# Kernel optimization log

Hardware: AMD Instinct MI355X
Metric: run time of the kernel (lower is better)

Reference implementation:

```python
import jax, jax.numpy as jnp
import numpy as np

N1, N2 = 8192, 8192
E1, E2 = 131072, 131072
F_IN, NH, B = 64, 128, 256
D6 = 6 * NH  # set2set in_channels = 768


def _gcn(x, W, b, src, dst, ew, n):
    xw = x @ W
    loop = jnp.arange(n)
    s = jnp.concatenate([src, loop])
    d = jnp.concatenate([dst, loop])
    w = jnp.concatenate([ew, jnp.ones((n,), ew.dtype)])
    deg = jax.ops.segment_sum(w, d, num_segments=n)
    dinv = jnp.where(deg > 0, jax.lax.rsqrt(deg), 0.0)
    norm = (dinv[s] * w * dinv[d])[:, None]
    return jax.ops.segment_sum(xw[s] * norm, d, num_segments=n) + b


def _leaky(x):
    return jax.nn.leaky_relu(x, 0.2)


def _l2norm(x):
    return x / jnp.maximum(jnp.linalg.norm(x, axis=1, keepdims=True), 1e-12)


def _set2set(x, batch, nseg, Wih, Whh, bih, bhh, steps=2):
    # Set2Set pooling: LSTM(input=2d, hidden=d) + segment softmax attention
    d = x.shape[1]
    h = jnp.zeros((nseg, d), x.dtype)
    c = jnp.zeros((nseg, d), x.dtype)
    q_star = jnp.zeros((nseg, 2 * d), x.dtype)
    for _ in range(steps):
        gates = q_star @ Wih.T + h @ Whh.T + bih + bhh
        gi, gf, gg, go = jnp.split(gates, 4, axis=1)  # torch LSTM gate order i,f,g,o
        c = jax.nn.sigmoid(gf) * c + jax.nn.sigmoid(gi) * jnp.tanh(gg)
        h = jax.nn.sigmoid(go) * jnp.tanh(c)
        e = jnp.sum(x * h[batch], axis=1)
        emax = jax.ops.segment_max(e, batch, num_segments=nseg)
        ee = jnp.exp(e - emax[batch])
        a = ee / jax.ops.segment_sum(ee, batch, num_segments=nseg)[batch]
        r = jax.ops.segment_sum(a[:, None] * x, batch, num_segments=nseg)
        q_star = jnp.concatenate([h, r], axis=1)
    return q_star


def setup_inputs():
    key = jax.random.key(0)
    ks = jax.random.split(key, 20)
    f32 = jnp.float32

    def xav(k, shp):
        fan_in, fan_out = shp[-1], shp[0] if len(shp) == 2 else shp[-1]
        lim = float(np.sqrt(6.0 / (shp[0] + shp[1])))
        return jax.random.uniform(k, shp, f32, -lim, lim)

    inp = {}
    inp["features_1"] = jax.random.normal(ks[0], (N1, F_IN), f32)
    inp["features_2"] = jax.random.normal(ks[1], (N2, F_IN), f32)
    inp["edge_attr_1"] = jax.random.uniform(ks[2], (E1,), f32)
    inp["edge_attr_2"] = jax.random.uniform(ks[3], (E2,), f32)
    inp["W0"] = xav(ks[4], (F_IN, NH)); inp["b0"] = jnp.zeros((NH,), f32)
    inp["W1"] = xav(ks[5], (NH, NH)); inp["b1"] = jnp.zeros((NH,), f32)
    inp["W2"] = xav(ks[6], (NH, NH)); inp["b2"] = jnp.zeros((NH,), f32)
    inp["Wih"] = xav(ks[7], (4 * D6, 2 * D6)); inp["bih"] = jnp.zeros((4 * D6,), f32)
    inp["Whh"] = xav(ks[8], (4 * D6, D6)); inp["bhh"] = jnp.zeros((4 * D6,), f32)
    inp["Wp1"] = xav(ks[9], (256, 4 * D6)); inp["bp1"] = jnp.zeros((256,), f32)
    inp["Wp2"] = xav(ks[10], (128, 256)); inp["bp2"] = jnp.zeros((128,), f32)
    inp["Wp3"] = xav(ks[11], (1, 128)); inp["bp3"] = jnp.zeros((1,), f32)
    inp["edge_index_1"] = jax.random.randint(ks[12], (2, E1), 0, N1)
    inp["edge_index_2"] = jax.random.randint(ks[13], (2, E2), 0, N2)
    inp["batch_1"] = jnp.sort(jax.random.randint(ks[14], (N1,), 0, B))
    inp["batch_2"] = jnp.sort(jax.random.randint(ks[15], (N2,), 0, B))
    return inp


def reference(features_1, features_2, edge_attr_1, edge_attr_2,
              W0, b0, W1, b1, W2, b2, Wih, bih, Whh, bhh,
              Wp1, bp1, Wp2, bp2, Wp3, bp3,
              edge_index_1, edge_index_2, batch_1, batch_2):
    s1, d1 = edge_index_1[0], edge_index_1[1]
    s2, d2 = edge_index_2[0], edge_index_2[1]

    f1a = _leaky(_gcn(features_1, W0, b0, s1, d1, edge_attr_1, N1))
    f2a = _leaky(_gcn(features_2, W0, b0, s2, d2, edge_attr_2, N2))
    f1b = _leaky(_gcn(f1a, W1, b1, s1, d1, edge_attr_1, N1))
    f2b = _leaky(_gcn(f2a, W1, b1, s2, d2, edge_attr_2, N2))
    f1c = _leaky(_gcn(f1b, W2, b2, s1, d1, edge_attr_1, N1))
    f2c = _leaky(_gcn(f2b, W2, b2, s2, d2, edge_attr_2, N2))
    h1 = jnp.concatenate([f1a, f1b, f1c], axis=1)  # [N1, 3*NH]
    h2 = jnp.concatenate([f2a, f2b, f2c], axis=1)  # [N2, 3*NH]

    # interaction: cosine-sim map masked to same-graph pairs (len_map)
    ns = _l2norm(h1)
    nv = _l2norm(h2)
    mask = (batch_1[:, None] == batch_2[None, :]).astype(ns.dtype)  # [N1, N2]
    imap = (ns @ nv.T) * mask
    f1 = jnp.concatenate([ns, imap @ nv], axis=1)      # [N1, 6*NH]
    f2 = jnp.concatenate([nv, imap.T @ ns], axis=1)    # [N2, 6*NH]

    g1 = _set2set(f1, batch_1, B, Wih, Whh, bih, bhh)  # [B, 12*NH]
    g2 = _set2set(f2, batch_2, B, Wih, Whh, bih, bhh)  # [B, 12*NH]
    z = jnp.concatenate([g1, g2], axis=1)              # [B, 24*NH]
    z = jax.nn.relu(z @ Wp1.T + bp1)
    z = jax.nn.relu(z @ Wp2.T + bp2)
    z = z @ Wp3.T + bp3
    return jax.nn.sigmoid(z).reshape(-1)
```

## Files before the change

kernel.cpp:

```cpp
#include <hip/hip_runtime.h>
#include <cmath>

#define N_NODES 8192
#define N_EDGES 131072
#define NB      256
#define NH      128
#define D3      384
#define D6      768
#define SMM     96

typedef __attribute__((ext_vector_type(8))) short short8v;
typedef __attribute__((ext_vector_type(4))) float f32x4;
typedef unsigned short bf16t;

__device__ __forceinline__ float sigf(float x){ return 1.0f/(1.0f+__expf(-x)); }
__device__ __forceinline__ unsigned short f2bf(float x){
  unsigned u = __float_as_uint(x);
  unsigned r = u + 0x7FFF + ((u>>16)&1);
  return (unsigned short)(r>>16);
}
__device__ __forceinline__ float bfl(unsigned u){ return __uint_as_float(u<<16); }
__device__ __forceinline__ float bfh(unsigned u){ return __uint_as_float(u & 0xFFFF0000u); }
__device__ __forceinline__ float b2f(bf16t u){ return __uint_as_float(((unsigned)u)<<16); }
__device__ __forceinline__ float h0val(const float* bih, const float* bhh, int j){
  float c = sigf(bih[j]+bhh[j]) * tanhf(bih[2*D6+j]+bhh[2*D6+j]);
  return sigf(bih[3*D6+j]+bhh[3*D6+j]) * tanhf(c);
}


__global__ void k_init(float* deg1, float* deg2, int* ecnt1, int* ecnt2, int* cnt1, int* cnt2){
  int t = blockIdx.x*blockDim.x + threadIdx.x;
  if (t < N_NODES){ deg1[t]=1.f; deg2[t]=1.f; ecnt1[t]=0; ecnt2[t]=0; }
  if (t < NB){ cnt1[t]=0; cnt2[t]=0; }
}

__global__ void k_deg(const int* __restrict__ ei1, const float* __restrict__ ea1, float* deg1, int* ecnt1,
                      const int* __restrict__ ei2, const float* __restrict__ ea2, float* deg2, int* ecnt2,
                      const int* __restrict__ b1, const int* __restrict__ b2, int* cnt1, int* cnt2){
  int idx = blockIdx.x*blockDim.x + threadIdx.x;
  int side = idx >= N_EDGES;
  int e = idx & (N_EDGES-1);
  const int* ei = side? ei2:ei1; const float* ea = side? ea2:ea1;
  float* deg = side? deg2:deg1;  int* ecnt = side? ecnt2:ecnt1;
  int d = ei[N_EDGES+e];
  atomicAdd(&deg[d], ea[e]);
  atomicAdd(&ecnt[d], 1);
  if (idx < N_NODES){ atomicAdd(&cnt1[b1[idx]],1); atomicAdd(&cnt2[b2[idx]],1); }
}

__global__ __launch_bounds__(256) void k_scan256(const int* c1, const int* c2, int* s1, int* s2){
  const int* c = blockIdx.x? c2:c1; int* st = blockIdx.x? s2:s1;
  __shared__ int ps[256];
  int t = threadIdx.x;
  ps[t]=c[t]; __syncthreads();
  for (int d=1; d<256; d<<=1){
    int v = (t>=d)? ps[t-d]:0;
    __syncthreads();
    ps[t]+=v;
    __syncthreads();
  }
  st[t+1]=ps[t];
  if (t==0) st[0]=0;
}

__global__ __launch_bounds__(1024) void k_escan(const int* ec1, const int* ec2,
                                                int* off1, int* cur1, int* off2, int* cur2){
  const int* cnt = blockIdx.x? ec2:ec1;
  int* off = blockIdx.x? off2:off1;
  int* cur = blockIdx.x? cur2:cur1;
  __shared__ int ps[1024];
  int t = threadIdx.x;
  int base = t*8;
  int loc[8]; int s=0;
  #pragma unroll
  for (int k=0;k<8;k++){ loc[k]=s; s+=cnt[base+k]; }
  ps[t]=s; __syncthreads();
  for (int d=1; d<1024; d<<=1){
    int v = (t>=d)? ps[t-d]:0;
    __syncthreads();
    ps[t]+=v;
    __syncthreads();
  }
  int pre = (t==0)? 0 : ps[t-1];
  #pragma unroll
  for (int k=0;k<8;k++){ int v=pre+loc[k]; off[base+k]=v; cur[base+k]=v; }
  if (t==1023) off[N_NODES]=ps[1023];
}

__global__ void k_fill(const int* __restrict__ ei1, const float* __restrict__ ea1, const float* __restrict__ d1,
                       int* cur1, int* es1, float* ec1,
                       const int* __restrict__ ei2, const float* __restrict__ ea2, const float* __restrict__ d2,
                       int* cur2, int* es2, float* ec2){
  int idx = blockIdx.x*blockDim.x + threadIdx.x;
  int side = idx >= N_EDGES;
  int e = idx & (N_EDGES-1);
  const int* ei = side? ei2:ei1; const float* ea = side? ea2:ea1;
  const float* deg = side? d2:d1;
  int* cur = side? cur2:cur1; int* es = side? es2:es1; float* ec = side? ec2:ec1;
  int s = ei[e], d = ei[N_EDGES+e];
  int pos = atomicAdd(&cur[d], 1);
  es[pos] = s;
  ec[pos] = rsqrtf(deg[s])*ea[e]*rsqrtf(deg[d]);
}

__global__ __launch_bounds__(256) void k_setup(
    const float* __restrict__ Wih, short* __restrict__ Wih16,
    const float* __restrict__ Wp1, short* __restrict__ Wp116,
    const float* __restrict__ fe1, const float* __restrict__ fe2,
    short* __restrict__ xf1, short* __restrict__ xf2,
    const float* __restrict__ W0, const float* __restrict__ W1, const float* __restrict__ W2,
    bf16t* __restrict__ Wt, uint4* __restrict__ Sz,
    const float* __restrict__ Whh, const float* __restrict__ bih, const float* __restrict__ bhh,
    float* __restrict__ cvec){
  __shared__ float hs[D6];
  int b = blockIdx.x, tid = threadIdx.x;
  if (b < 2304){
    int t = b*256 + tid;
    int n = t/192, q = t - n*192;
    float4 v = ((const float4*)(Wih + (size_t)n*1536 + 768))[q];
    short4 o = { (short)f2bf(v.x), (short)f2bf(v.y), (short)f2bf(v.z), (short)f2bf(v.w) };
    ((short4*)Wih16)[t] = o;
  } else if (b < 3072){
    int t = (b-2304)*256 + tid;
    float4 v = ((const float4*)Wp1)[t];
    short4 o = { (short)f2bf(v.x), (short)f2bf(v.y), (short)f2bf(v.z), (short)f2bf(v.w) };
    ((short4*)Wp116)[t] = o;
  } else if (b < 4096){
    int t = (b-3072)*256 + tid;
    int side = t >= 131072; int i = t & 131071;
    float4 v = ((const float4*)(side? fe2:fe1))[i];
    short4 o = { (short)f2bf(v.x), (short)f2bf(v.y), (short)f2bf(v.z), (short)f2bf(v.w) };
    ((short4*)(side? xf2:xf1))[i] = o;
  } else if (b < 6400){
    Sz[(size_t)(b-4096)*256 + tid] = make_uint4(0,0,0,0);
  } else if (b < 6403){
    int l = b - 6400;
    const float* W = (l==0)? W0 : ((l==1)? W1 : W2);
    int K = (l==0)? 64 : 128;
    bf16t* dst = Wt + ((l==0)? 0 : ((l==1)? 128*64 : 128*64+128*128));
    for (int idx = tid; idx < 128*K; idx += 256){
      int n = idx / K, k = idx - n*K;
      dst[idx] = f2bf(W[k*NH + n]);
    }
  } else {
    int j0 = (b - 6403)*4;
    for (int k=tid; k<D6; k+=256) hs[k] = h0val(bih,bhh,k);
    __syncthreads();
    int w = tid>>6, lane = tid&63;
    int j = j0 + w;
    const float4* wi = (const float4*)(Wih + (size_t)j*(2*D6));
    const float4* wh = (const float4*)(Whh + (size_t)j*D6);
    const float4* h4 = (const float4*)hs;
    float acc=0;
    #pragma unroll
    for (int m=0;m<3;m++){
      float4 hv = h4[m*64+lane];
      float4 a = wi[m*64+lane];
      float4 bb = wh[m*64+lane];
      acc += hv.x*(a.x+bb.x) + hv.y*(a.y+bb.y) + hv.z*(a.z+bb.z) + hv.w*(a.w+bb.w);
    }
    #pragma unroll
    for (int m=1;m<64;m<<=1) acc += __shfl_xor(acc,m,64);
    if (lane==0) cvec[j]=acc+bih[j]+bhh[j];
  }
}


__global__ __launch_bounds__(256) void k_xw_mfma(const bf16t* __restrict__ x1, const bf16t* __restrict__ x2,
                                                 int xs, int K, const bf16t* __restrict__ Wt,
                                                 bf16t* __restrict__ xw1, bf16t* __restrict__ xw2){
  int blk = blockIdx.x;
  int side = blk >> 8; int b = blk & 255;
  const bf16t* x = side? x2:x1;
  bf16t* xw = side? xw2:xw1;
  int w = threadIdx.x>>6, lane = threadIdx.x&63;
  int lm = lane&15, quad = lane>>4;
  int r0 = b*32 + (w>>1)*16;
  int c0 = (w&1)*64;
  const bf16t* a = x + (size_t)(r0+lm)*xs + quad*8;
  f32x4 acc[4] = {};
  for (int k=0;k<K;k+=32){
    short8v af = *(const short8v*)(a + k);
    #pragma unroll
    for (int ni=0;ni<4;ni++){
      short8v bf = *(const short8v*)(Wt + (size_t)(c0+ni*16+lm)*K + quad*8 + k);
      acc[ni] = __builtin_amdgcn_mfma_f32_16x16x32_bf16(af, bf, acc[ni], 0,0,0);
    }
  }
  #pragma unroll
  for (int ni=0;ni<4;ni++)
    #pragma unroll
    for (int r=0;r<4;r++){
      int row = r0 + quad*4 + r, col = c0 + ni*16 + lm;
      xw[(size_t)row*NH + col] = f2bf(acc[ni][r]);
    }
}

__global__ __launch_bounds__(256) void k_gather(const bf16t* __restrict__ xw1, const bf16t* __restrict__ xw2,
                                                const int* __restrict__ off1, const int* __restrict__ off2,
                                                const int* __restrict__ es1, const int* __restrict__ es2,
                                                const float* __restrict__ ec1, const float* __restrict__ ec2,
                                                const float* __restrict__ d1, const float* __restrict__ d2,
                                                const float* __restrict__ b,
                                                bf16t* __restrict__ h1, bf16t* __restrict__ h2, int loff,
                                                int l2mode, bf16t* __restrict__ f1, bf16t* __restrict__ f2){
  int blk = blockIdx.x;
  int side = blk >> 10; int bb = blk & 1023;
  const ushort4* xw = (const ushort4*)(side? xw2:xw1);
  const int* off = side? off2:off1;
  const int* es  = side? es2:es1;
  const float* ec= side? ec2:ec1;
  const float* deg = side? d2:d1;
  bf16t* h = side? h2:h1;
  int t = threadIdx.x;
  int i = bb*8 + (t>>5);
  int c4 = t & 31;
  float sc = 1.0f/deg[i];
  ushort4 v = xw[(size_t)i*32 + c4];
  float4 acc = {b2f(v.x)*sc, b2f(v.y)*sc, b2f(v.z)*sc, b2f(v.w)*sc};
  int r = off[i], r1 = off[i+1];
  for (; r+3<r1; r+=4){
    int s0=es[r], s1=es[r+1], s2=es[r+2], s3=es[r+3];
    float w0=ec[r], w1=ec[r+1], w2=ec[r+2], w3=ec[r+3];
    ushort4 u0 = xw[(size_t)s0*32 + c4];
    ushort4 u1 = xw[(size_t)s1*32 + c4];
    ushort4 u2 = xw[(size_t)s2*32 + c4];
    ushort4 u3 = xw[(size_t)s3*32 + c4];
    acc.x += b2f(u0.x)*w0 + b2f(u1.x)*w1 + b2f(u2.x)*w2 + b2f(u3.x)*w3;
    acc.y += b2f(u0.y)*w0 + b2f(u1.y)*w1 + b2f(u2.y)*w2 + b2f(u3.y)*w3;
    acc.z += b2f(u0.z)*w0 + b2f(u1.z)*w1 + b2f(u2.z)*w2 + b2f(u3.z)*w3;
    acc.w += b2f(u0.w)*w0 + b2f(u1.w)*w1 + b2f(u2.w)*w2 + b2f(u3.w)*w3;
  }
  for (; r<r1; r++){
    int s0=es[r]; float w0=ec[r];
    ushort4 u0 = xw[(size_t)s0*32 + c4];
    acc.x+=b2f(u0.x)*w0; acc.y+=b2f(u0.y)*w0; acc.z+=b2f(u0.z)*w0; acc.w+=b2f(u0.w)*w0;
  }
  float4 bv = ((const float4*)b)[c4];
  acc.x+=bv.x; acc.y+=bv.y; acc.z+=bv.z; acc.w+=bv.w;
  acc.x = (acc.x>0.f)?acc.x:0.2f*acc.x;
  acc.y = (acc.y>0.f)?acc.y:0.2f*acc.y;
  acc.z = (acc.z>0.f)?acc.z:0.2f*acc.z;
  acc.w = (acc.w>0.f)?acc.w:0.2f*acc.w;
  if (!l2mode){
    ((ushort4*)(h + (size_t)i*D3 + loff))[c4] =
      make_ushort4(f2bf(acc.x), f2bf(acc.y), f2bf(acc.z), f2bf(acc.w));
  } else {
    ushort4 u0 = ((const ushort4*)(h + (size_t)i*D3))[c4];
    ushort4 u1 = ((const ushort4*)(h + (size_t)i*D3 + 128))[c4];
    float4 v0 = {b2f(u0.x), b2f(u0.y), b2f(u0.z), b2f(u0.w)};
    float4 v1 = {b2f(u1.x), b2f(u1.y), b2f(u1.z), b2f(u1.w)};
    float ss = v0.x*v0.x+v0.y*v0.y+v0.z*v0.z+v0.w*v0.w
             + v1.x*v1.x+v1.y*v1.y+v1.z*v1.z+v1.w*v1.w
             + acc.x*acc.x+acc.y*acc.y+acc.z*acc.z+acc.w*acc.w;
    #pragma unroll
    for (int m=1;m<32;m<<=1) ss += __shfl_xor(ss, m, 64);
    float scale = 1.0f/fmaxf(sqrtf(ss), 1e-12f);
    bf16t* f = side? f2:f1;
    ((ushort4*)(f + (size_t)i*D6))[c4]       = make_ushort4(f2bf(v0.x*scale),f2bf(v0.y*scale),f2bf(v0.z*scale),f2bf(v0.w*scale));
    ((ushort4*)(f + (size_t)i*D6 + 128))[c4] = make_ushort4(f2bf(v1.x*scale),f2bf(v1.y*scale),f2bf(v1.z*scale),f2bf(v1.w*scale));
    ((ushort4*)(f + (size_t)i*D6 + 256))[c4] = make_ushort4(f2bf(acc.x*scale),f2bf(acc.y*scale),f2bf(acc.z*scale),f2bf(acc.w*scale));
  }
}

__global__ __launch_bounds__(256) void k_smat(const bf16t* __restrict__ f1, const bf16t* __restrict__ f2,
                                              const int* __restrict__ st1, const int* __restrict__ st2,
                                              bf16t* __restrict__ S, bf16t* __restrict__ ST){
  int g = blockIdx.x;
  int it2 = blockIdx.y/3, jt2 = blockIdx.y - it2*3;
  int i0 = st1[g]; int n1 = st1[g+1]-i0; if (n1>SMM) n1=SMM;
  int j0 = st2[g]; int n2 = st2[g+1]-j0; if (n2>SMM) n2=SMM;
  if (it2*32 >= n1 || jt2*32 >= n2) return;
  int w = threadIdx.x >> 6, lane = threadIdx.x & 63;
  int lm = lane & 15, quad = lane >> 4;
  int ti = it2*2 + (w>>1), tj = jt2*2 + (w&1);
  if (ti*16 >= n1 || tj*16 >= n2) return;
  const bf16t* a = f1 + (size_t)(i0 + ti*16 + lm)*D6 + quad*8;
  const bf16t* b = f2 + (size_t)(j0 + tj*16 + lm)*D6 + quad*8;
  f32x4 acc = {0,0,0,0};
  #pragma unroll
  for (int k=0; k<384; k+=32){
    short8v af = *(const short8v*)(a + k);
    short8v bf = *(const short8v*)(b + k);
    acc = __builtin_amdgcn_mfma_f32_16x16x32_bf16(af, bf, acc, 0, 0, 0);
  }
  bf16t* Sg  = S  + (size_t)g*SMM*SMM;
  bf16t* STg = ST + (size_t)g*SMM*SMM;
  int col = tj*16 + lm;
  #pragma unroll
  for (int r=0;r<4;r++){
    int row = ti*16 + quad*4 + r;
    if (row < n1 && col < n2){
      bf16t v = f2bf(acc[r]);
      Sg [(size_t)row*SMM + col] = v;
      STg[(size_t)col*SMM + row] = v;
    }
  }
}

__global__ __launch_bounds__(256) void k_apply(bf16t* __restrict__ f1, bf16t* __restrict__ f2,
                                               const int* __restrict__ st1, const int* __restrict__ st2,
                                               const bf16t* __restrict__ S, const bf16t* __restrict__ ST){
  __shared__ bf16t tbuf[32*392];
  int bx = blockIdx.x;
  int side = bx >> 8, g = bx & (NB-1);
  int a0 = st1[g]; int n1 = st1[g+1]-a0; if (n1>SMM) n1=SMM;
  int b0 = st2[g]; int n2 = st2[g+1]-b0; if (n2>SMM) n2=SMM;
  int cnt = side? n2 : n1;
  int J   = side? n1 : n2;
  int r0 = blockIdx.y*32;
  if (r0 >= cnt) return;
  const bf16t* src = side? (f1 + (size_t)a0*D6) : (f2 + (size_t)b0*D6);
  bf16t* dst = (side? (f2 + (size_t)b0*D6) : (f1 + (size_t)a0*D6)) + D3;
  const bf16t* Sg = (side? ST : S) + (size_t)g*SMM*SMM;
  int t = threadIdx.x, w = t>>6, lane = t&63;
  int lm = lane & 15, quad = lane >> 4;
  int mt1 = (cnt - r0 > 16) ? 2 : 1;
  f32x4 acc[2][6] = {};
  for (int kb = 0; kb < J; kb += 32){
    __syncthreads();
    for (int idx = t; idx < 32*48; idx += 256){
      int j = idx/48, cg = idx - j*48;
      uint4 v = (kb+j < J)? ((const uint4*)(src + (size_t)(kb+j)*D6))[cg] : make_uint4(0,0,0,0);
      *(uint4*)(tbuf + j*392 + cg*8) = v;
    }
    short8v af0, af1;
    {
      const bf16t* ap = Sg + (size_t)(r0 + lm)*SMM + kb + quad*8;
      af0 = *(const short8v*)ap;
      af1 = (mt1 > 1)? *(const short8v*)(ap + 16*SMM) : af0;
    }
    __syncthreads();
    #pragma unroll
    for (int ni = 0; ni < 6; ni++){
      int nt = w*6 + ni;
      short8v bf;
      #pragma unroll
      for (int ji = 0; ji < 8; ji++)
        bf[ji] = (short)tbuf[(quad*8 + ji)*392 + nt*16 + lm];
      acc[0][ni] = __builtin_amdgcn_mfma_f32_16x16x32_bf16(af0, bf, acc[0][ni], 0, 0, 0);
      if (mt1 > 1)
        acc[1][ni] = __builtin_amdgcn_mfma_f32_16x16x32_bf16(af1, bf, acc[1][ni], 0, 0, 0);
    }
  }
  for (int mt = 0; mt < mt1; mt++)
    for (int ni = 0; ni < 6; ni++){
      int nt = w*6 + ni;
      #pragma unroll
      for (int r = 0; r < 4; r++){
        int row = r0 + mt*16 + quad*4 + r;
        if (row < cnt) dst[(size_t)row*D6 + nt*16 + lm] = f2bf(acc[mt][ni][r]);
      }
    }
}


__global__ __launch_bounds__(256) void k_att(const bf16t* __restrict__ f1, const bf16t* __restrict__ f2,
                                             const float* __restrict__ hbase, int perseg,
                                             const float* __restrict__ bih, const float* __restrict__ bhh,
                                             const int* __restrict__ st1, const int* __restrict__ st2,
                                             bf16t* __restrict__ dst16, long sidestep, long dstride){
  __shared__ float4 hs[192];
  __shared__ float e_s[SMM];
  __shared__ float part[4][D6];
  int side = blockIdx.x >> 8, g = blockIdx.x & (NB-1);
  const int* st = side? st2:st1;
  int n0 = st[g]; int cnt = st[g+1]-n0; if (cnt>SMM) cnt=SMM;
  const bf16t* x = (side? f2:f1) + (size_t)n0*D6;
  int t = threadIdx.x, w = t>>6, lane = t&63;
  if (t<192){
    if (perseg){
      hs[t] = ((const float4*)(hbase + (size_t)(side*NB+g)*D6))[t];
    } else {
      int j = t*4;
      hs[t] = make_float4(h0val(bih,bhh,j), h0val(bih,bhh,j+1), h0val(bih,bhh,j+2), h0val(bih,bhh,j+3));
    }
  }
  __syncthreads();
  for (int n=w; n<cnt; n+=4){
    const uint2* xr = (const uint2*)(x + (size_t)n*D6);
    float p = 0;
    #pragma unroll
    for (int m=0;m<3;m++){
      uint2 rv = xr[m*64+lane];
      float4 hvv = hs[m*64+lane];
      p += bfl(rv.x)*hvv.x + bfh(rv.x)*hvv.y + bfl(rv.y)*hvv.z + bfh(rv.y)*hvv.w;
    }
    #pragma unroll
    for (int m=1;m<64;m<<=1) p += __shfl_xor(p,m,64);
    if (lane==0) e_s[n]=p;
  }
  __syncthreads();
  if (w==0){
    float mx=-INFINITY;
    for (int n=lane;n<cnt;n+=64) mx=fmaxf(mx,e_s[n]);
    #pragma unroll
    for (int m=1;m<64;m<<=1) mx=fmaxf(mx,__shfl_xor(mx,m,64));
    float s=0;
    for (int n=lane;n<cnt;n+=64) s+=__expf(e_s[n]-mx);
    #pragma unroll
    for (int m=1;m<64;m<<=1) s+=__shfl_xor(s,m,64);
    float inv=1.0f/s;
    for (int n=lane;n<cnt;n+=64) e_s[n]=__expf(e_s[n]-mx)*inv;
  }
  __syncthreads();
  float av[3][4] = {};
  for (int n=w; n<cnt; n+=4){
    float a = e_s[n];
    const uint2* xr = (const uint2*)(x + (size_t)n*D6);
    #pragma unroll
    for (int m=0;m<3;m++){
      uint2 rv = xr[m*64+lane];
      av[m][0]+=a*bfl(rv.x); av[m][1]+=a*bfh(rv.x); av[m][2]+=a*bfl(rv.y); av[m][3]+=a*bfh(rv.y);
    }
  }
  #pragma unroll
  for (int m=0;m<3;m++)
    *(float4*)&part[w][(m*64+lane)*4] = make_float4(av[m][0],av[m][1],av[m][2],av[m][3]);
  __syncthreads();
  if (t<192){
    float4 p0 = *(const float4*)&part[0][t*4];
    float4 p1 = *(const float4*)&part[1][t*4];
    float4 p2 = *(const float4*)&part[2][t*4];
    float4 p3 = *(const float4*)&part[3][t*4];
    float4 s = make_float4(p0.x+p1.x+p2.x+p3.x, p0.y+p1.y+p2.y+p3.y,
                           p0.z+p1.z+p2.z+p3.z, p0.w+p1.w+p2.w+p3.w);
    ushort4 o = make_ushort4(f2bf(s.x), f2bf(s.y), f2bf(s.z), f2bf(s.w));
    ((ushort4*)(dst16 + side*sidestep + (size_t)g*dstride))[t]=o;
  }
}

__global__ __launch_bounds__(256) void k_gemm_mfma(const short* __restrict__ A16,
                                                   const short* __restrict__ B16,
                                                   float* __restrict__ pout){
  int w = threadIdx.x >> 6, lane = threadIdx.x & 63;
  int lm = lane & 15, quad = lane >> 4;
  int bm = blockIdx.x * 16;
  int bn = blockIdx.y * 256 + w * 64;
  const short* a = A16 + (size_t)(bm + lm)*768 + quad*8;
  const short* b = B16 + (size_t)(bn + lm)*768 + quad*8;
  f32x4 acc0={0,0,0,0}, acc1={0,0,0,0}, acc2={0,0,0,0}, acc3={0,0,0,0};
  for (int k=0; k<768; k+=32){
    short8v af = *(const short8v*)(a + k);
    short8v b0 = *(const short8v*)(b + k);
    short8v b1 = *(const short8v*)(b + 16*768 + k);
    short8v b2 = *(const short8v*)(b + 32*768 + k);
    short8v b3 = *(const short8v*)(b + 48*768 + k);
    acc0 = __builtin_amdgcn_mfma_f32_16x16x32_bf16(af, b0, acc0, 0, 0, 0);
    acc1 = __builtin_amdgcn_mfma_f32_16x16x32_bf16(af, b1, acc1, 0, 0, 0);
    acc2 = __builtin_amdgcn_mfma_f32_16x16x32_bf16(af, b2, acc2, 0, 0, 0);
    acc3 = __builtin_amdgcn_mfma_f32_16x16x32_bf16(af, b3, acc3, 0, 0, 0);
  }
  #pragma unroll
  for (int r=0;r<4;r++){
    size_t base = (size_t)(bm + quad*4 + r)*3072 + bn + lm;
    pout[base]      = acc0[r];
    pout[base + 16] = acc1[r];
    pout[base + 32] = acc2[r];
    pout[base + 48] = acc3[r];
  }
}

__global__ __launch_bounds__(256) void k_gemm_mfma_p1(const short* __restrict__ A16,
                                                      const short* __restrict__ B16,
                                                      float* __restrict__ pout){
  int w = threadIdx.x >> 6, lane = threadIdx.x & 63;
  int lm = lane & 15, quad = lane >> 4;
  int bm = blockIdx.x * 16;
  int bn = w * 64;
  int kbase = blockIdx.y * 192;
  const short* a = A16 + (size_t)(bm + lm)*3072 + quad*8 + kbase;
  const short* b = B16 + (size_t)(bn + lm)*3072 + quad*8 + kbase;
  f32x4 acc0={0,0,0,0}, acc1={0,0,0,0}, acc2={0,0,0,0}, acc3={0,0,0,0};
  for (int k=0; k<192; k+=32){
    short8v af = *(const short8v*)(a + k);
    short8v b0 = *(const short8v*)(b + k);
    short8v b1 = *(const short8v*)(b + 16*3072 + k);
    short8v b2 = *(const short8v*)(b + 32*3072 + k);
    short8v b3 = *(const short8v*)(b + 48*3072 + k);
    acc0 = __builtin_amdgcn_mfma_f32_16x16x32_bf16(af, b0, acc0, 0, 0, 0);
    acc1 = __builtin_amdgcn_mfma_f32_16x16x32_bf16(af, b1, acc1, 0, 0, 0);
    acc2 = __builtin_amdgcn_mfma_f32_16x16x32_bf16(af, b2, acc2, 0, 0, 0);
    acc3 = __builtin_amdgcn_mfma_f32_16x16x32_bf16(af, b3, acc3, 0, 0, 0);
  }
  float* po = pout + (size_t)blockIdx.y*256*256;
  #pragma unroll
  for (int r=0;r<4;r++){
    size_t base = (size_t)(bm + quad*4 + r)*256 + bn + lm;
    po[base]      = acc0[r];
    po[base + 16] = acc1[r];
    po[base + 32] = acc2[r];
    po[base + 48] = acc3[r];
  }
}

__global__ __launch_bounds__(256) void k_lstm_red(const float* __restrict__ pbuf,
                                                  const float* __restrict__ cvec,
                                                  const float* __restrict__ bih, const float* __restrict__ bhh,
                                                  float* __restrict__ h1s, bf16t* __restrict__ z16){
  int t = blockIdx.x*256 + threadIdx.x;
  int m = t/D6, j = t - m*D6;
  const float* p0 = pbuf + (size_t)m*3072 + j;
  float g4[4];
  #pragma unroll
  for (int q=0;q<4;q++) g4[q] = cvec[q*D6 + j] + p0[q*D6];
  float c0j = sigf(bih[j]+bhh[j]) * tanhf(bih[2*D6+j]+bhh[2*D6+j]);
  float c = sigf(g4[1])*c0j + sigf(g4[0])*tanhf(g4[2]);
  float h = sigf(g4[3])*tanhf(c);
  h1s[(size_t)m*D6 + j] = h;
  int side = m>>8, g = m&255;
  z16[(size_t)g*3072 + side*1536 + j] = f2bf(h);
}

__global__ __launch_bounds__(128) void k_p23(const float* __restrict__ pbuf, const float* __restrict__ bp1,
                                             const float* __restrict__ Wp2, const float* __restrict__ bp2,
                                             const float* __restrict__ Wp3, const float* __restrict__ bp3,
                                             float* __restrict__ out){
  __shared__ float zr[256];
  __shared__ float ws[2];
  int m = blockIdx.x, t = threadIdx.x;
  float2 zacc = ((const float2*)(bp1))[t];
  #pragma unroll
  for (int p=0;p<16;p++){
    float2 v = ((const float2*)(pbuf + (size_t)p*256*256 + (size_t)m*256))[t];
    zacc.x += v.x; zacc.y += v.y;
  }
  zr[2*t]   = fmaxf(zacc.x, 0.f);
  zr[2*t+1] = fmaxf(zacc.y, 0.f);
  __syncthreads();
  const float4* wrow = (const float4*)(Wp2 + (size_t)t*256);
  const float4* z4 = (const float4*)zr;
  float acc = bp2[t];
  #pragma unroll 8
  for (int k=0;k<64;k++){
    float4 wv = wrow[k], zv = z4[k];
    acc += wv.x*zv.x + wv.y*zv.y + wv.z*zv.z + wv.w*zv.w;
  }
  float p = fmaxf(acc,0.f)*Wp3[t];
  #pragma unroll
  for (int o=32;o;o>>=1) p += __shfl_down(p,o,64);
  if ((t&63)==0) ws[t>>6]=p;
  __syncthreads();
  if (t==0){ float v=ws[0]+ws[1]+bp3[0]; out[m]=1.0f/(1.0f+__expf(-v)); }
}


extern "C" void kernel_launch(void* const* d_in, const int* in_sizes, int n_in,
                              void* d_out, int out_size, void* d_ws, size_t ws_size,
                              hipStream_t stream){
  const float* feat1=(const float*)d_in[0];
  const float* feat2=(const float*)d_in[1];
  const float* ea1  =(const float*)d_in[2];
  const float* ea2  =(const float*)d_in[3];
  const float* W0=(const float*)d_in[4];  const float* b0=(const float*)d_in[5];
  const float* W1=(const float*)d_in[6];  const float* b1=(const float*)d_in[7];
  const float* W2=(const float*)d_in[8];  const float* b2=(const float*)d_in[9];
  const float* Wih=(const float*)d_in[10]; const float* bih=(const float*)d_in[11];
  const float* Whh=(const float*)d_in[12]; const float* bhh=(const float*)d_in[13];
  const float* Wp1=(const float*)d_in[14]; const float* bp1=(const float*)d_in[15];
  const float* Wp2=(const float*)d_in[16]; const float* bp2=(const float*)d_in[17];
  const float* Wp3=(const float*)d_in[18]; const float* bp3=(const float*)d_in[19];
  const int* ei1=(const int*)d_in[20]; const int* ei2=(const int*)d_in[21];
  const int* batch1=(const int*)d_in[22]; const int* batch2=(const int*)d_in[23];
  float* out = (float*)d_out;

  float* base = (float*)d_ws;
  size_t off = 0;
  auto alloc = [&](size_t n)->float* { float* r = base + off; off += (n + 255) & ~(size_t)255; return r; };
  float* deg1 = alloc(N_NODES);          float* deg2 = alloc(N_NODES);
  bf16t* xw1  = (bf16t*)alloc((size_t)N_NODES*NH/2);
  bf16t* xw2  = (bf16t*)alloc((size_t)N_NODES*NH/2);
  bf16t* hb1  = (bf16t*)alloc((size_t)N_NODES*D3/2);
  bf16t* hb2  = (bf16t*)alloc((size_t)N_NODES*D3/2);
  bf16t* xf1  = (bf16t*)alloc((size_t)N_NODES*64/2);
  bf16t* xf2  = (bf16t*)alloc((size_t)N_NODES*64/2);
  bf16t* Wtb  = (bf16t*)alloc((size_t)(128*64 + 2*128*128)/2);
  bf16t* f1   = (bf16t*)alloc((size_t)N_NODES*D6/2);
  bf16t* f2   = (bf16t*)alloc((size_t)N_NODES*D6/2);
  float* ecoef1 = alloc(N_EDGES);        float* ecoef2 = alloc(N_EDGES);
  float* cvec = alloc(4*D6);
  bf16t* Sbuf = (bf16t*)alloc((size_t)NB*SMM*SMM);
  bf16t* STbuf= Sbuf + (size_t)NB*SMM*SMM;
  float* h1s  = alloc((size_t)512*D6);
  bf16t* zbuf16 = (bf16t*)alloc((size_t)256*3072/2);
  float* pbuf = alloc((size_t)4*512*3072);
  short* Abuf16 = (short*)alloc((size_t)512*D6/2);
  short* Wih16  = (short*)alloc((size_t)3072*D6/2);
  short* Wp116  = (short*)alloc((size_t)256*3072/2);
  int* cnt1 = (int*)alloc(NB);   int* cnt2 = (int*)alloc(NB);
  int* st1  = (int*)alloc(NB+1); int* st2  = (int*)alloc(NB+1);
  int* ecnt1= (int*)alloc(N_NODES); int* ecnt2 = (int*)alloc(N_NODES);
  int* eoff1= (int*)alloc(N_NODES+1); int* eoff2 = (int*)alloc(N_NODES+1);
  int* ecur1= (int*)alloc(N_NODES); int* ecur2 = (int*)alloc(N_NODES);
  int* esrc1= (int*)alloc(N_EDGES); int* esrc2 = (int*)alloc(N_EDGES);
  (void)ws_size; (void)in_sizes; (void)n_in; (void)out_size;

  k_init   <<<32,256,0,stream>>>(deg1,deg2,ecnt1,ecnt2,cnt1,cnt2);
  k_deg    <<<1024,256,0,stream>>>(ei1,ea1,deg1,ecnt1, ei2,ea2,deg2,ecnt2, batch1,batch2,cnt1,cnt2);
  k_scan256<<<2,256,0,stream>>>(cnt1,cnt2,st1,st2);
  k_escan  <<<2,1024,0,stream>>>(ecnt1,ecnt2,eoff1,ecur1,eoff2,ecur2);
  k_fill   <<<1024,256,0,stream>>>(ei1,ea1,deg1,ecur1,esrc1,ecoef1, ei2,ea2,deg2,ecur2,esrc2,ecoef2);
  k_setup  <<<7171,256,0,stream>>>(Wih,Wih16, Wp1,Wp116, feat1,feat2,(short*)xf1,(short*)xf2,
                                   W0,W1,W2,Wtb, (uint4*)Sbuf, Whh,bih,bhh, cvec);

  const float* bs[3]={b0,b1,b2};
  const bf16t* Wts[3]={Wtb, Wtb+128*64, Wtb+128*64+128*128};
  for (int l=0;l<3;l++){
    const bf16t* x1 = (l==0)? xf1 : (hb1 + (l-1)*NH);
    const bf16t* x2 = (l==0)? xf2 : (hb2 + (l-1)*NH);
    int xs = (l==0)? 64 : D3;
    int K  = (l==0)? 64 : NH;
    k_xw_mfma<<<512,256,0,stream>>>(x1,x2,xs,K,Wts[l],xw1,xw2);
    k_gather <<<2048,256,0,stream>>>(xw1,xw2,eoff1,eoff2,esrc1,esrc2,ecoef1,ecoef2,
                                     deg1,deg2,bs[l],hb1,hb2,l*NH,(l==2)?1:0,f1,f2);
  }

  k_smat  <<<dim3(256,9),256,0,stream>>>(f1,f2,st1,st2,Sbuf,STbuf);
  k_apply <<<dim3(512,3),256,0,stream>>>(f1,f2,st1,st2,Sbuf,STbuf);

  k_att<<<512,256,0,stream>>>(f1,f2,(const float*)nullptr,0,bih,bhh,st1,st2,
                              (bf16t*)Abuf16,(long)256*D6,(long)D6);

  k_gemm_mfma<<<dim3(32,12),256,0,stream>>>(Abuf16, Wih16, pbuf);
  k_lstm_red <<<1536,256,0,stream>>>(pbuf,cvec,bih,bhh,h1s,zbuf16);

  k_att<<<512,256,0,stream>>>(f1,f2,h1s,1,bih,bhh,st1,st2,
                              zbuf16+768,(long)1536,(long)3072);

  k_gemm_mfma_p1<<<dim3(16,16),256,0,stream>>>((const short*)zbuf16, Wp116, pbuf);
  k_p23 <<<256,128,0,stream>>>(pbuf, bp1, Wp2, bp2, Wp3, bp3, out);
}
```

Before: 357.0 us.

## Fuse similarity and apply kernels, gates GEMM with LSTM, and setup launches

The per-graph similarity matrix is now computed into LDS and applied in the same kernel, for both sides. This drops the global S/ST buffers and the pass that zeroed them. The LSTM gate nonlinearity is applied in the GEMM epilogue through shared memory, so the full fp32 gate buffer is no longer written and reread. The init kernel is folded into the setup kernel and the two scans are merged into one launch, cutting launch count. The risk is that the fused interaction kernel runs only 256 blocks and handles both sides serially, so it has much less parallelism than the old split kernels.

```diff
diff --git a/kernel.cpp b/kernel.cpp
--- a/kernel.cpp
+++ b/kernel.cpp
@@ -8,6 +8,7 @@
 #define D3      384
 #define D6      768
 #define SMM     96
+#define SLD     104
 
 typedef __attribute__((ext_vector_type(8))) short short8v;
 typedef __attribute__((ext_vector_type(4))) float f32x4;
@@ -27,12 +28,6 @@
   return sigf(bih[3*D6+j]+bhh[3*D6+j]) * tanhf(c);
 }
 
-
-__global__ void k_init(float* deg1, float* deg2, int* ecnt1, int* ecnt2, int* cnt1, int* cnt2){
-  int t = blockIdx.x*blockDim.x + threadIdx.x;
-  if (t < N_NODES){ deg1[t]=1.f; deg2[t]=1.f; ecnt1[t]=0; ecnt2[t]=0; }
-  if (t < NB){ cnt1[t]=0; cnt2[t]=0; }
-}
 
 __global__ void k_deg(const int* __restrict__ ei1, const float* __restrict__ ea1, float* deg1, int* ecnt1,
                       const int* __restrict__ ei2, const float* __restrict__ ea2, float* deg2, int* ecnt2,
@@ -48,43 +43,43 @@
   if (idx < N_NODES){ atomicAdd(&cnt1[b1[idx]],1); atomicAdd(&cnt2[b2[idx]],1); }
 }
 
-__global__ __launch_bounds__(256) void k_scan256(const int* c1, const int* c2, int* s1, int* s2){
-  const int* c = blockIdx.x? c2:c1; int* st = blockIdx.x? s2:s1;
-  __shared__ int ps[256];
-  int t = threadIdx.x;
-  ps[t]=c[t]; __syncthreads();
-  for (int d=1; d<256; d<<=1){
-    int v = (t>=d)? ps[t-d]:0;
+__global__ __launch_bounds__(1024) void k_scans(const int* ec1, const int* ec2,
+                                                int* off1, int* cur1, int* off2, int* cur2,
+                                                const int* c1, const int* c2, int* s1, int* s2){
+  __shared__ int ps[1024];
+  int bx = blockIdx.x, t = threadIdx.x;
+  if (bx < 2){
+    const int* cnt = bx? ec2:ec1;
+    int* off = bx? off2:off1;
+    int* cur = bx? cur2:cur1;
+    int base = t*8;
+    int loc[8]; int s=0;
+    #pragma unroll
+    for (int k=0;k<8;k++){ loc[k]=s; s+=cnt[base+k]; }
+    ps[t]=s; __syncthreads();
+    for (int d=1; d<1024; d<<=1){
+      int v = (t>=d)? ps[t-d]:0;
+      __syncthreads();
+      ps[t]+=v;
+      __syncthreads();
+    }
+    int pre = (t==0)? 0 : ps[t-1];
+    #pragma unroll
+    for (int k=0;k<8;k++){ int v=pre+loc[k]; off[base+k]=v; cur[base+k]=v; }
+    if (t==1023) off[N_NODES]=ps[1023];
+  } else {
+    const int* c = (bx==3)? c2:c1; int* st = (bx==3)? s2:s1;
+    ps[t] = (t<256)? c[t] : 0;
     __syncthreads();
-    ps[t]+=v;
-    __syncthreads();
-  }
-  st[t+1]=ps[t];
-  if (t==0) st[0]=0;
-}
-
-__global__ __launch_bounds__(1024) void k_escan(const int* ec1, const int* ec2,
-                                                int* off1, int* cur1, int* off2, int* cur2){
-  const int* cnt = blockIdx.x? ec2:ec1;
-  int* off = blockIdx.x? off2:off1;
-  int* cur = blockIdx.x? cur2:cur1;
-  __shared__ int ps[1024];
-  int t = threadIdx.x;
-  int base = t*8;
-  int loc[8]; int s=0;
-  #pragma unroll
-  for (int k=0;k<8;k++){ loc[k]=s; s+=cnt[base+k]; }
-  ps[t]=s; __syncthreads();
-  for (int d=1; d<1024; d<<=1){
-    int v = (t>=d)? ps[t-d]:0;
-    __syncthreads();
-    ps[t]+=v;
-    __syncthreads();
-  }
-  int pre = (t==0)? 0 : ps[t-1];
-  #pragma unroll
-  for (int k=0;k<8;k++){ int v=pre+loc[k]; off[base+k]=v; cur[base+k]=v; }
-  if (t==1023) off[N_NODES]=ps[1023];
+    for (int d=1; d<256; d<<=1){
+      int v = (t>=d)? ps[t-d]:0;
+      __syncthreads();
+      ps[t]+=v;
+      __syncthreads();
+    }
+    if (t<256) st[t+1]=ps[t];
+    if (t==0) st[0]=0;
+  }
 }
 
 __global__ void k_fill(const int* __restrict__ ei1, const float* __restrict__ ea1, const float* __restrict__ d1,
@@ -109,9 +104,10 @@
     const float* __restrict__ fe1, const float* __restrict__ fe2,
     short* __restrict__ xf1, short* __restrict__ xf2,
     const float* __restrict__ W0, const float* __restrict__ W1, const float* __restrict__ W2,
-    bf16t* __restrict__ Wt, uint4* __restrict__ Sz,
+    bf16t* __restrict__ Wt,
     const float* __restrict__ Whh, const float* __restrict__ bih, const float* __restrict__ bhh,
-    float* __restrict__ cvec){
+    float* __restrict__ cvec,
+    float* deg1, float* deg2, int* ecnt1, int* ecnt2, int* cnt1, int* cnt2){
   __shared__ float hs[D6];
   int b = blockIdx.x, tid = threadIdx.x;
   if (b < 2304){
@@ -131,10 +127,8 @@
     float4 v = ((const float4*)(side? fe2:fe1))[i];
     short4 o = { (short)f2bf(v.x), (short)f2bf(v.y), (short)f2bf(v.z), (short)f2bf(v.w) };
     ((short4*)(side? xf2:xf1))[i] = o;
-  } else if (b < 6400){
-    Sz[(size_t)(b-4096)*256 + tid] = make_uint4(0,0,0,0);
-  } else if (b < 6403){
-    int l = b - 6400;
+  } else if (b < 4099){
+    int l = b - 4096;
     const float* W = (l==0)? W0 : ((l==1)? W1 : W2);
     int K = (l==0)? 64 : 128;
     bf16t* dst = Wt + ((l==0)? 0 : ((l==1)? 128*64 : 128*64+128*128));
@@ -142,8 +136,8 @@
       int n = idx / K, k = idx - n*K;
       dst[idx] = f2bf(W[k*NH + n]);
     }
-  } else {
-    int j0 = (b - 6403)*4;
+  } else if (b < 4867){
+    int j0 = (b - 4099)*4;
     for (int k=tid; k<D6; k+=256) hs[k] = h0val(bih,bhh,k);
     __syncthreads();
     int w = tid>>6, lane = tid&63;
@@ -162,6 +156,10 @@
     #pragma unroll
     for (int m=1;m<64;m<<=1) acc += __shfl_xor(acc,m,64);
     if (lane==0) cvec[j]=acc+bih[j]+bhh[j];
+  } else {
+    int t = (b-4867)*256 + tid;
+    if (t < N_NODES){ deg1[t]=1.f; deg2[t]=1.f; ecnt1[t]=0; ecnt2[t]=0; }
+    if (t < NB){ cnt1[t]=0; cnt2[t]=0; }
   }
 }
 
@@ -263,95 +261,91 @@
   }
 }
 
-__global__ __launch_bounds__(256) void k_smat(const bf16t* __restrict__ f1, const bf16t* __restrict__ f2,
-                                              const int* __restrict__ st1, const int* __restrict__ st2,
-                                              bf16t* __restrict__ S, bf16t* __restrict__ ST){
+__global__ __launch_bounds__(256) void k_inter(bf16t* __restrict__ f1, bf16t* __restrict__ f2,
+                                               const int* __restrict__ st1, const int* __restrict__ st2){
+  __shared__ bf16t Sld[SMM*SLD];
+  __shared__ bf16t STld[SMM*SLD];
+  __shared__ bf16t tbuf[32*392];
   int g = blockIdx.x;
-  int it2 = blockIdx.y/3, jt2 = blockIdx.y - it2*3;
   int i0 = st1[g]; int n1 = st1[g+1]-i0; if (n1>SMM) n1=SMM;
   int j0 = st2[g]; int n2 = st2[g+1]-j0; if (n2>SMM) n2=SMM;
-  if (it2*32 >= n1 || jt2*32 >= n2) return;
-  int w = threadIdx.x >> 6, lane = threadIdx.x & 63;
-  int lm = lane & 15, quad = lane >> 4;
-  int ti = it2*2 + (w>>1), tj = jt2*2 + (w&1);
-  if (ti*16 >= n1 || tj*16 >= n2) return;
-  const bf16t* a = f1 + (size_t)(i0 + ti*16 + lm)*D6 + quad*8;
-  const bf16t* b = f2 + (size_t)(j0 + tj*16 + lm)*D6 + quad*8;
-  f32x4 acc = {0,0,0,0};
-  #pragma unroll
-  for (int k=0; k<384; k+=32){
-    short8v af = *(const short8v*)(a + k);
-    short8v bf = *(const short8v*)(b + k);
-    acc = __builtin_amdgcn_mfma_f32_16x16x32_bf16(af, bf, acc, 0, 0, 0);
-  }
-  bf16t* Sg  = S  + (size_t)g*SMM*SMM;
-  bf16t* STg = ST + (size_t)g*SMM*SMM;
-  int col = tj*16 + lm;
-  #pragma unroll
-  for (int r=0;r<4;r++){
-    int row = ti*16 + quad*4 + r;
-    if (row < n1 && col < n2){
-      bf16t v = f2bf(acc[r]);
-      Sg [(size_t)row*SMM + col] = v;
-      STg[(size_t)col*SMM + row] = v;
-    }
-  }
-}
-
-__global__ __launch_bounds__(256) void k_apply(bf16t* __restrict__ f1, bf16t* __restrict__ f2,
-                                               const int* __restrict__ st1, const int* __restrict__ st2,
-                                               const bf16t* __restrict__ S, const bf16t* __restrict__ ST){
-  __shared__ bf16t tbuf[32*392];
-  int bx = blockIdx.x;
-  int side = bx >> 8, g = bx & (NB-1);
-  int a0 = st1[g]; int n1 = st1[g+1]-a0; if (n1>SMM) n1=SMM;
-  int b0 = st2[g]; int n2 = st2[g+1]-b0; if (n2>SMM) n2=SMM;
-  int cnt = side? n2 : n1;
-  int J   = side? n1 : n2;
-  int r0 = blockIdx.y*32;
-  if (r0 >= cnt) return;
-  const bf16t* src = side? (f1 + (size_t)a0*D6) : (f2 + (size_t)b0*D6);
-  bf16t* dst = (side? (f2 + (size_t)b0*D6) : (f1 + (size_t)a0*D6)) + D3;
-  const bf16t* Sg = (side? ST : S) + (size_t)g*SMM*SMM;
   int t = threadIdx.x, w = t>>6, lane = t&63;
   int lm = lane & 15, quad = lane >> 4;
-  int mt1 = (cnt - r0 > 16) ? 2 : 1;
-  f32x4 acc[2][6] = {};
-  for (int kb = 0; kb < J; kb += 32){
-    __syncthreads();
-    for (int idx = t; idx < 32*48; idx += 256){
-      int j = idx/48, cg = idx - j*48;
-      uint4 v = (kb+j < J)? ((const uint4*)(src + (size_t)(kb+j)*D6))[cg] : make_uint4(0,0,0,0);
-      *(uint4*)(tbuf + j*392 + cg*8) = v;
-    }
-    short8v af0, af1;
-    {
-      const bf16t* ap = Sg + (size_t)(r0 + lm)*SMM + kb + quad*8;
-      af0 = *(const short8v*)ap;
-      af1 = (mt1 > 1)? *(const short8v*)(ap + 16*SMM) : af0;
-    }
-    __syncthreads();
-    #pragma unroll
-    for (int ni = 0; ni < 6; ni++){
-      int nt = w*6 + ni;
-      short8v bf;
-      #pragma unroll
-      for (int ji = 0; ji < 8; ji++)
-        bf[ji] = (short)tbuf[(quad*8 + ji)*392 + nt*16 + lm];
-      acc[0][ni] = __builtin_amdgcn_mfma_f32_16x16x32_bf16(af0, bf, acc[0][ni], 0, 0, 0);
-      if (mt1 > 1)
-        acc[1][ni] = __builtin_amdgcn_mfma_f32_16x16x32_bf16(af1, bf, acc[1][ni], 0, 0, 0);
-    }
-  }
-  for (int mt = 0; mt < mt1; mt++)
-    for (int ni = 0; ni < 6; ni++){
-      int nt = w*6 + ni;
-      #pragma unroll
-      for (int r = 0; r < 4; r++){
-        int row = r0 + mt*16 + quad*4 + r;
-        if (row < cnt) dst[(size_t)row*D6 + nt*16 + lm] = f2bf(acc[mt][ni][r]);
+  {
+    uint4* z1 = (uint4*)Sld; uint4* z2 = (uint4*)STld;
+    uint4 zz = make_uint4(0,0,0,0);
+    for (int i=t; i<1248; i+=256){ z1[i]=zz; z2[i]=zz; }
+  }
+  __syncthreads();
+  int nti = (n1+15)>>4, ntj = (n2+15)>>4;
+  for (int tile = w; tile < nti*ntj; tile += 4){
+    int ti = tile/ntj, tj = tile - ti*ntj;
+    int ar = i0 + ti*16 + lm; if (ar > N_NODES-1) ar = N_NODES-1;
+    int br = j0 + tj*16 + lm; if (br > N_NODES-1) br = N_NODES-1;
+    const bf16t* a = f1 + (size_t)ar*D6 + quad*8;
+    const bf16t* b = f2 + (size_t)br*D6 + quad*8;
+    f32x4 acc = {0,0,0,0};
+    #pragma unroll
+    for (int k=0; k<384; k+=32){
+      short8v af = *(const short8v*)(a + k);
+      short8v bf = *(const short8v*)(b + k);
+      acc = __builtin_amdgcn_mfma_f32_16x16x32_bf16(af, bf, acc, 0, 0, 0);
+    }
+    int col = tj*16 + lm;
+    #pragma unroll
+    for (int r=0;r<4;r++){
+      int row = ti*16 + quad*4 + r;
+      if (row < n1 && col < n2){
+        bf16t v = f2bf(acc[r]);
+        Sld [row*SLD + col] = v;
+        STld[col*SLD + row] = v;
       }
     }
+  }
+  __syncthreads();
+  for (int side=0; side<2; side++){
+    int cnt = side? n2 : n1;
+    int J   = side? n1 : n2;
+    const bf16t* src = side? (f1 + (size_t)i0*D6) : (f2 + (size_t)j0*D6);
+    bf16t* dst = (side? (f2 + (size_t)j0*D6) : (f1 + (size_t)i0*D6)) + D3;
+    const bf16t* Sm = side? STld : Sld;
+    for (int r0=0; r0<cnt; r0+=32){
+      int mt1 = (cnt - r0 > 16) ? 2 : 1;
+      f32x4 acc[2][6] = {};
+      for (int kb = 0; kb < J; kb += 32){
+        __syncthreads();
+        for (int idx = t; idx < 32*48; idx += 256){
+          int j = idx/48, cg = idx - j*48;
+          uint4 v = (kb+j < J)? ((const uint4*)(src + (size_t)(kb+j)*D6))[cg] : make_uint4(0,0,0,0);
+          *(uint4*)(tbuf + j*392 + cg*8) = v;
+        }
+        const bf16t* ap = Sm + (r0 + lm)*SLD + kb + quad*8;
+        short8v af0 = *(const short8v*)ap;
+        short8v af1 = (mt1 > 1)? *(const short8v*)(ap + 16*SLD) : af0;
+        __syncthreads();
+        #pragma unroll
+        for (int ni = 0; ni < 6; ni++){
+          int nt = w*6 + ni;
+          short8v bf;
+          #pragma unroll
+          for (int ji = 0; ji < 8; ji++)
+            bf[ji] = (short)tbuf[(quad*8 + ji)*392 + nt*16 + lm];
+          acc[0][ni] = __builtin_amdgcn_mfma_f32_16x16x32_bf16(af0, bf, acc[0][ni], 0, 0, 0);
+          if (mt1 > 1)
+            acc[1][ni] = __builtin_amdgcn_mfma_f32_16x16x32_bf16(af1, bf, acc[1][ni], 0, 0, 0);
+        }
+      }
+      for (int mt = 0; mt < mt1; mt++)
+        for (int ni = 0; ni < 6; ni++){
+          int nt = w*6 + ni;
+          #pragma unroll
+          for (int r = 0; r < 4; r++){
+            int row = r0 + mt*16 + quad*4 + r;
+            if (row < cnt) dst[(size_t)row*D6 + nt*16 + lm] = f2bf(acc[mt][ni][r]);
+          }
+        }
+    }
+  }
 }
 
 
@@ -430,15 +424,18 @@
   }
 }
 
-__global__ __launch_bounds__(256) void k_gemm_mfma(const short* __restrict__ A16,
-                                                   const short* __restrict__ B16,
-                                                   float* __restrict__ pout){
+__global__ __launch_bounds__(256) void k_gates(const short* __restrict__ A16,
+                                               const short* __restrict__ B16,
+                                               const float* __restrict__ cvec,
+                                               const float* __restrict__ bih, const float* __restrict__ bhh,
+                                               float* __restrict__ h1s, bf16t* __restrict__ z16){
+  __shared__ float gbuf[4][16][66];
   int w = threadIdx.x >> 6, lane = threadIdx.x & 63;
   int lm = lane & 15, quad = lane >> 4;
   int bm = blockIdx.x * 16;
-  int bn = blockIdx.y * 256 + w * 64;
+  int jb = blockIdx.y * 64;
   const short* a = A16 + (size_t)(bm + lm)*768 + quad*8;
-  const short* b = B16 + (size_t)(bn + lm)*768 + quad*8;
+  const short* b = B16 + (size_t)(w*768 + jb + lm)*768 + quad*8;
   f32x4 acc0={0,0,0,0}, acc1={0,0,0,0}, acc2={0,0,0,0}, acc3={0,0,0,0};
   for (int k=0; k<768; k+=32){
     short8v af = *(const short8v*)(a + k);
@@ -453,11 +450,27 @@
   }
   #pragma unroll
   for (int r=0;r<4;r++){
-    size_t base = (size_t)(bm + quad*4 + r)*3072 + bn + lm;
-    pout[base]      = acc0[r];
-    pout[base + 16] = acc1[r];
-    pout[base + 32] = acc2[r];
-    pout[base + 48] = acc3[r];
+    gbuf[w][quad*4+r][lm]      = acc0[r];
+    gbuf[w][quad*4+r][16+lm]   = acc1[r];
+    gbuf[w][quad*4+r][32+lm]   = acc2[r];
+    gbuf[w][quad*4+r][48+lm]   = acc3[r];
+  }
+  __syncthreads();
+  int t = threadIdx.x;
+  #pragma unroll
+  for (int u=0; u<4; u++){
+    int p = t + u*256;
+    int mm = p>>6, jj = p&63;
+    int j = jb + jj, m = bm + mm;
+    float g4[4];
+    #pragma unroll
+    for (int q=0;q<4;q++) g4[q] = gbuf[q][mm][jj] + cvec[q*D6 + j];
+    float c0j = sigf(bih[j]+bhh[j]) * tanhf(bih[2*D6+j]+bhh[2*D6+j]);
+    float c = sigf(g4[1])*c0j + sigf(g4[0])*tanhf(g4[2]);
+    float h = sigf(g4[3])*tanhf(c);
+    h1s[(size_t)m*D6 + j] = h;
+    int side = m>>8, g = m&255;
+    z16[(size_t)g*3072 + side*1536 + j] = f2bf(h);
   }
 }
 
@@ -494,24 +507,6 @@
   }
 }
 
-__global__ __launch_bounds__(256) void k_lstm_red(const float* __restrict__ pbuf,
-                                                  const float* __restrict__ cvec,
-                                                  const float* __restrict__ bih, const float* __restrict__ bhh,
-                                                  float* __restrict__ h1s, bf16t* __restrict__ z16){
-  int t = blockIdx.x*256 + threadIdx.x;
-  int m = t/D6, j = t - m*D6;
-  const float* p0 = pbuf + (size_t)m*3072 + j;
-  float g4[4];
-  #pragma unroll
-  for (int q=0;q<4;q++) g4[q] = cvec[q*D6 + j] + p0[q*D6];
-  float c0j = sigf(bih[j]+bhh[j]) * tanhf(bih[2*D6+j]+bhh[2*D6+j]);
-  float c = sigf(g4[1])*c0j + sigf(g4[0])*tanhf(g4[2]);
-  float h = sigf(g4[3])*tanhf(c);
-  h1s[(size_t)m*D6 + j] = h;
-  int side = m>>8, g = m&255;
-  z16[(size_t)g*3072 + side*1536 + j] = f2bf(h);
-}
-
 __global__ __launch_bounds__(128) void k_p23(const float* __restrict__ pbuf, const float* __restrict__ bp1,
                                              const float* __restrict__ Wp2, const float* __restrict__ bp2,
                                              const float* __restrict__ Wp3, const float* __restrict__ bp3,
@@ -579,11 +574,9 @@
   bf16t* f2   = (bf16t*)alloc((size_t)N_NODES*D6/2);
   float* ecoef1 = alloc(N_EDGES);        float* ecoef2 = alloc(N_EDGES);
   float* cvec = alloc(4*D6);
-  bf16t* Sbuf = (bf16t*)alloc((size_t)NB*SMM*SMM);
-  bf16t* STbuf= Sbuf + (size_t)NB*SMM*SMM;
   float* h1s  = alloc((size_t)512*D6);
   bf16t* zbuf16 = (bf16t*)alloc((size_t)256*3072/2);
-  float* pbuf = alloc((size_t)4*512*3072);
+  float* pbuf = alloc((size_t)16*256*256);
   short* Abuf16 = (short*)alloc((size_t)512*D6/2);
   short* Wih16  = (short*)alloc((size_t)3072*D6/2);
   short* Wp116  = (short*)alloc((size_t)256*3072/2);
@@ -595,13 +588,12 @@
   int* esrc1= (int*)alloc(N_EDGES); int* esrc2 = (int*)alloc(N_EDGES);
   (void)ws_size; (void)in_sizes; (void)n_in; (void)out_size;
 
-  k_init   <<<32,256,0,stream>>>(deg1,deg2,ecnt1,ecnt2,cnt1,cnt2);
+  k_setup  <<<4899,256,0,stream>>>(Wih,Wih16, Wp1,Wp116, feat1,feat2,(short*)xf1,(short*)xf2,
+                                   W0,W1,W2,Wtb, Whh,bih,bhh, cvec,
+                                   deg1,deg2,ecnt1,ecnt2,cnt1,cnt2);
   k_deg    <<<1024,256,0,stream>>>(ei1,ea1,deg1,ecnt1, ei2,ea2,deg2,ecnt2, batch1,batch2,cnt1,cnt2);
-  k_scan256<<<2,256,0,stream>>>(cnt1,cnt2,st1,st2);
-  k_escan  <<<2,1024,0,stream>>>(ecnt1,ecnt2,eoff1,ecur1,eoff2,ecur2);
+  k_scans  <<<4,1024,0,stream>>>(ecnt1,ecnt2,eoff1,ecur1,eoff2,ecur2, cnt1,cnt2,st1,st2);
   k_fill   <<<1024,256,0,stream>>>(ei1,ea1,deg1,ecur1,esrc1,ecoef1, ei2,ea2,deg2,ecur2,esrc2,ecoef2);
-  k_setup  <<<7171,256,0,stream>>>(Wih,Wih16, Wp1,Wp116, feat1,feat2,(short*)xf1,(short*)xf2,
-                                   W0,W1,W2,Wtb, (uint4*)Sbuf, Whh,bih,bhh, cvec);
 
   const float* bs[3]={b0,b1,b2};
   const bf16t* Wts[3]={Wtb, Wtb+128*64, Wtb+128*64+128*128};
@@ -615,14 +607,12 @@
                                      deg1,deg2,bs[l],hb1,hb2,l*NH,(l==2)?1:0,f1,f2);
   }
 
-  k_smat  <<<dim3(256,9),256,0,stream>>>(f1,f2,st1,st2,Sbuf,STbuf);
-  k_apply <<<dim3(512,3),256,0,stream>>>(f1,f2,st1,st2,Sbuf,STbuf);
+  k_inter <<<256,256,0,stream>>>(f1,f2,st1,st2);
 
   k_att<<<512,256,0,stream>>>(f1,f2,(const float*)nullptr,0,bih,bhh,st1,st2,
                               (bf16t*)Abuf16,(long)256*D6,(long)D6);
 
-  k_gemm_mfma<<<dim3(32,12),256,0,stream>>>(Abuf16, Wih16, pbuf);
-  k_lstm_red <<<1536,256,0,stream>>>(pbuf,cvec,bih,bhh,h1s,zbuf16);
+  k_gates<<<dim3(32,12),256,0,stream>>>(Abuf16, Wih16, cvec, bih, bhh, h1s, zbuf16);
 
   k_att<<<512,256,0,stream>>>(f1,f2,h1s,1,bih,bhh,st1,st2,
                               zbuf16+768,(long)1536,(long)3072);
```

After: 360.7 us. Within noise of the previous version (+1.1%).
